# Kernel optimization log

Hardware: AMD Instinct MI355X
Metric: run time of the kernel (lower is better)

The kernel has to match this reference:

```python
import jax, jax.numpy as jnp
import numpy as np
from jax import lax

N, T, H, E = 50000, 200, 128, 1600000


def setup_inputs() -> dict:
    key = jax.random.key(0)
    ks = jax.random.split(key, 32)
    s = 0.05
    inp = {}
    inp["lightcurve"] = jax.random.normal(ks[0], (N, T), dtype=jnp.float32)
    inp["edge_index"] = jax.random.randint(ks[1], (2, E), 0, N, dtype=jnp.int32)
    # LSTM layer 0 (input_dim=1) and layer 1 (input H), PyTorch gate order i,f,g,o
    inp["W_ih0"] = jax.random.normal(ks[2], (4 * H, 1), jnp.float32) * s
    inp["W_hh0"] = jax.random.normal(ks[3], (4 * H, H), jnp.float32) * s
    inp["b_ih0"] = jnp.zeros((4 * H,), jnp.float32)
    inp["b_hh0"] = jnp.zeros((4 * H,), jnp.float32)
    inp["W_ih1"] = jax.random.normal(ks[4], (4 * H, H), jnp.float32) * s
    inp["W_hh1"] = jax.random.normal(ks[5], (4 * H, H), jnp.float32) * s
    inp["b_ih1"] = jnp.zeros((4 * H,), jnp.float32)
    inp["b_hh1"] = jnp.zeros((4 * H,), jnp.float32)
    # 3 GCN conv layers + LayerNorms
    for i in range(3):
        inp[f"Wg{i}"] = jax.random.normal(ks[6 + i], (H, H), jnp.float32) * s
        inp[f"bg{i}"] = jnp.zeros((H,), jnp.float32)
        inp[f"gamma{i}"] = jnp.ones((H,), jnp.float32)
        inp[f"beta{i}"] = jnp.zeros((H,), jnp.float32)
    inp["W_out"] = jax.random.normal(ks[10], (H, 1), jnp.float32) * s
    inp["b_out"] = jnp.zeros((1,), jnp.float32)
    return inp


def _lstm_encode(x, W_ih0, W_hh0, b_ih0, b_hh0, W_ih1, W_hh1, b_ih1, b_hh1):
    # x: [N, T, 1] -> final hidden of layer 2: [N, H]. Both layers fused in one scan.
    n = x.shape[0]
    h = W_hh0.shape[1]

    def cell(xt, hs, cs, Wih, Whh, bih, bhh):
        g = xt @ Wih.T + hs @ Whh.T + (bih + bhh)
        i, f, gg, o = jnp.split(g, 4, axis=-1)
        cs = jax.nn.sigmoid(f) * cs + jax.nn.sigmoid(i) * jnp.tanh(gg)
        hs = jax.nn.sigmoid(o) * jnp.tanh(cs)
        return hs, cs

    def step(carry, x_t):
        h1, c1, h2, c2 = carry
        h1, c1 = cell(x_t, h1, c1, W_ih0, W_hh0, b_ih0, b_hh0)
        h2, c2 = cell(h1, h2, c2, W_ih1, W_hh1, b_ih1, b_hh1)
        return (h1, c1, h2, c2), None

    z = jnp.zeros((n, h), x.dtype)
    (_, _, h2, _), _ = lax.scan(step, (z, z, z, z), jnp.swapaxes(x, 0, 1))
    return h2


def _forward(lightcurve, W_ih0, W_hh0, b_ih0, b_hh0, W_ih1, W_hh1, b_ih1, b_hh1,
             Wg0, bg0, gamma0, beta0, Wg1, bg1, gamma1, beta1, Wg2, bg2, gamma2, beta2,
             W_out, b_out, edge_index):
    n = lightcurve.shape[0]
    h = _lstm_encode(lightcurve[..., None], W_ih0, W_hh0, b_ih0, b_hh0,
                     W_ih1, W_hh1, b_ih1, b_hh1)
    # GCN normalization (PyG GCNConv defaults: add self-loops, symmetric norm)
    loops = jnp.arange(n, dtype=edge_index.dtype)
    row = jnp.concatenate([edge_index[0], loops])  # source
    col = jnp.concatenate([edge_index[1], loops])  # target
    deg = jax.ops.segment_sum(jnp.ones_like(col, dtype=h.dtype), col, num_segments=n)
    dinv = lax.rsqrt(jnp.maximum(deg, 1.0))
    enorm = dinv[row] * dinv[col]  # [E+N]
    for Wg, bg, gm, bt in ((Wg0, bg0, gamma0, beta0), (Wg1, bg1, gamma1, beta1), (Wg2, bg2, gamma2, beta2)):
        h_prev = h
        msg = (h @ Wg)[row] * enorm[:, None]            # gather + scale
        h = jax.ops.segment_sum(msg, col, num_segments=n) + bg  # scatter-add
        mu = h.mean(-1, keepdims=True)                  # LayerNorm
        var = jnp.mean((h - mu) ** 2, axis=-1, keepdims=True)
        h = (h - mu) * lax.rsqrt(var + 1e-5) * gm + bt
        h = jax.nn.relu(h)
        h = h + h_prev  # dropout is identity in eval mode
    pooled = h.mean(axis=0, keepdims=True)  # [1, H]
    return pooled @ W_out + b_out           # [1, 1]


def reference(lightcurve, edge_index, W_ih0, W_hh0, b_ih0, b_hh0,
              W_ih1, W_hh1, b_ih1, b_hh1,
              Wg0, bg0, gamma0, beta0, Wg1, bg1, gamma1, beta1,
              Wg2, bg2, gamma2, beta2, W_out, b_out):
    return _forward(lightcurve, W_ih0, W_hh0, b_ih0, b_hh0, W_ih1, W_hh1, b_ih1, b_hh1,
                    Wg0, bg0, gamma0, beta0, Wg1, bg1, gamma1, beta1,
                    Wg2, bg2, gamma2, beta2, W_out, b_out, edge_index)
```

## Files before the change

kernel.cpp:

```cpp
#include <hip/hip_runtime.h>

#define NN 50000
#define TT 200
#define HH 128
#define EE 1600000

typedef _Float16 f16x8 __attribute__((ext_vector_type(8)));
typedef _Float16 f16x4 __attribute__((ext_vector_type(4)));
typedef __fp16 fp16x2 __attribute__((ext_vector_type(2)));
typedef float f32x4 __attribute__((ext_vector_type(4)));

__device__ __forceinline__ float sigf(float x) {
    return __builtin_amdgcn_rcpf(1.f + __expf(-x));
}
__device__ __forceinline__ float tanhf_(float x) {
    return 1.f - 2.f * __builtin_amdgcn_rcpf(__expf(2.f * x) + 1.f);
}
__device__ __forceinline__ f32x4 sig4(f32x4 x) {
    f32x4 r; r[0] = sigf(x[0]); r[1] = sigf(x[1]); r[2] = sigf(x[2]); r[3] = sigf(x[3]); return r;
}
__device__ __forceinline__ f32x4 tanh4(f32x4 x) {
    f32x4 r; r[0] = tanhf_(x[0]); r[1] = tanhf_(x[1]); r[2] = tanhf_(x[2]); r[3] = tanhf_(x[3]); return r;
}
__device__ __forceinline__ f32x4 splat4(float s) { f32x4 r = {s, s, s, s}; return r; }
__device__ __forceinline__ f16x4 pack4(f32x4 v) {
    struct P { fp16x2 lo, hi; } p;
    p.lo = __builtin_amdgcn_cvt_pkrtz(v[0], v[1]);
    p.hi = __builtin_amdgcn_cvt_pkrtz(v[2], v[3]);
    return __builtin_bit_cast(f16x4, p);
}

__global__ void pack_w(const float* __restrict__ W, _Float16* __restrict__ out) {
    int tile = blockIdx.x;
    int jn = tile >> 2, kk = tile & 3;
    int L = threadIdx.x;
    int n = jn * 16 + (L & 15);
    int k0 = kk * 32 + (L >> 4) * 8;
    _Float16* dst = out + (size_t)tile * 512 + L * 8;
#pragma unroll
    for (int i = 0; i < 8; ++i) dst[i] = (_Float16)W[n * 128 + k0 + i];
}

__global__ void bias_prep(const float* __restrict__ bih0, const float* __restrict__ bhh0,
                          const float* __restrict__ bih1, const float* __restrict__ bhh1,
                          const float* __restrict__ wih0,
                          float* __restrict__ b0g, float* __restrict__ b1g, float* __restrict__ wxg) {
    int i = blockIdx.x * 256 + threadIdx.x;
    if (i < 512) {
        b0g[i] = bih0[i] + bhh0[i];
        b1g[i] = bih1[i] + bhh1[i];
        wxg[i] = wih0[i];
    }
}

__global__ void transpose_lc(const float* __restrict__ lc, float* __restrict__ xT) {
    __shared__ float tile[32][33];
    int tx = threadIdx.x, ty = threadIdx.y;
    int n0 = blockIdx.y * 32, t0 = blockIdx.x * 32;
#pragma unroll
    for (int i = 0; i < 32; i += 8) {
        int n = n0 + ty + i, t = t0 + tx;
        if (n < NN && t < TT) tile[ty + i][tx] = lc[(size_t)n * TT + t];
    }
    __syncthreads();
#pragma unroll
    for (int i = 0; i < 32; i += 8) {
        int t = t0 + ty + i, n = n0 + tx;
        if (n < NN && t < TT) xT[(size_t)t * NN + n] = tile[tx][ty + i];
    }
}


#define MFMA16(A, B, C) __builtin_amdgcn_mfma_f32_16x16x32_f16((A), (B), (C), 0, 0, 0)

#define MMCW(WB, HR, KK) {                                                      \
    const _Float16* wb_ = (WB) + (size_t)(KK) * 512 + lane * 8;                 \
    f16x8 wI_ = *reinterpret_cast<const f16x8*>(wb_ + (size_t)(0 * 8 + wj) * 2048); \
    f16x8 wF_ = *reinterpret_cast<const f16x8*>(wb_ + (size_t)(1 * 8 + wj) * 2048); \
    f16x8 wG_ = *reinterpret_cast<const f16x8*>(wb_ + (size_t)(2 * 8 + wj) * 2048); \
    f16x8 wO_ = *reinterpret_cast<const f16x8*>(wb_ + (size_t)(3 * 8 + wj) * 2048); \
    f16x8 h0_ = *reinterpret_cast<const f16x8*>(&(HR)[col][(KK) * 32 + quad * 8]);      \
    f16x8 h1_ = *reinterpret_cast<const f16x8*>(&(HR)[16 + col][(KK) * 32 + quad * 8]); \
    aI0 = MFMA16(wI_, h0_, aI0); aI1 = MFMA16(wI_, h1_, aI1);                   \
    aF0 = MFMA16(wF_, h0_, aF0); aF1 = MFMA16(wF_, h1_, aF1);                   \
    aG0 = MFMA16(wG_, h0_, aG0); aG1 = MFMA16(wG_, h1_, aG1);                   \
    aO0 = MFMA16(wO_, h0_, aO0); aO1 = MFMA16(wO_, h1_, aO1);                   \
}

#define EPIL0(NT, C, HV, AI, AF, AG, AO, XB) {                                  \
    f32x4 bI_ = *reinterpret_cast<const f32x4*>(&b0s[j0]);                      \
    f32x4 bF_ = *reinterpret_cast<const f32x4*>(&b0s[128 + j0]);                \
    f32x4 bG_ = *reinterpret_cast<const f32x4*>(&b0s[256 + j0]);                \
    f32x4 bO_ = *reinterpret_cast<const f32x4*>(&b0s[384 + j0]);                \
    f32x4 wIv_ = *reinterpret_cast<const f32x4*>(&wxs[j0]);                     \
    f32x4 wFv_ = *reinterpret_cast<const f32x4*>(&wxs[128 + j0]);               \
    f32x4 wGv_ = *reinterpret_cast<const f32x4*>(&wxs[256 + j0]);               \
    f32x4 wOv_ = *reinterpret_cast<const f32x4*>(&wxs[384 + j0]);               \
    f32x4 xv_ = splat4(xs[XB][(NT) * 16 + col]);                                \
    f32x4 gi_ = AI + bI_ + xv_ * wIv_;                                          \
    f32x4 gf_ = AF + bF_ + xv_ * wFv_;                                          \
    f32x4 gg_ = AG + bG_ + xv_ * wGv_;                                          \
    f32x4 go_ = AO + bO_ + xv_ * wOv_;                                          \
    C = sig4(gf_) * C + sig4(gi_) * tanh4(gg_);                                 \
    HV = sig4(go_) * tanh4(C);                                                  \
}

#define EPIL1(NT, C, HV, AI, AF, AG, AO) {                                      \
    f32x4 bI_ = *reinterpret_cast<const f32x4*>(&b1s[j0]);                      \
    f32x4 bF_ = *reinterpret_cast<const f32x4*>(&b1s[128 + j0]);                \
    f32x4 bG_ = *reinterpret_cast<const f32x4*>(&b1s[256 + j0]);                \
    f32x4 bO_ = *reinterpret_cast<const f32x4*>(&b1s[384 + j0]);                \
    f32x4 gi_ = AI + bI_;                                                       \
    f32x4 gf_ = AF + bF_;                                                       \
    f32x4 gg_ = AG + bG_;                                                       \
    f32x4 go_ = AO + bO_;                                                       \
    C = sig4(gf_) * C + sig4(gi_) * tanh4(gg_);                                 \
    HV = sig4(go_) * tanh4(C);                                                  \
}

#define WRHV(DST, NT, HV) \
    *reinterpret_cast<f16x4*>(&(DST)[(NT) * 16 + col][j0]) = pack4(HV);

__global__ __launch_bounds__(512, 2) void lstm_kernel(
    const float* __restrict__ xT,
    const _Float16* __restrict__ w0p,
    const _Float16* __restrict__ w1ip,
    const _Float16* __restrict__ w1hp,
    const float* __restrict__ b0g, const float* __restrict__ b1g,
    const float* __restrict__ wxg,
    float* __restrict__ h2out) {
    __shared__ _Float16 h1s[2][32][136];
    __shared__ _Float16 h2s[2][32][136];
    __shared__ __align__(16) float xs[2][32];
    __shared__ __align__(16) float b0s[512], b1s[512], wxs[512];

    const int tid = threadIdx.x;
    const int w = tid >> 6;
    const int wj = __builtin_amdgcn_readfirstlane(w);
    const int lane = tid & 63;
    const int col = lane & 15;
    const int quad = lane >> 4;
    const int n0 = blockIdx.x * 32;
    const int j0 = wj * 16 + quad * 4;

    for (int i = tid; i < 32 * 136; i += 512) (&h2s[1][0][0])[i] = (_Float16)0;
    if (tid < 512) { b0s[tid] = b0g[tid]; b1s[tid] = b1g[tid]; wxs[tid] = wxg[tid]; }
    if (tid < 32) {
        int n = n0 + tid;
        xs[0][tid] = (n < NN) ? xT[n] : 0.f;
        xs[1][tid] = (n < NN) ? xT[(size_t)NN + n] : 0.f;
    }

    f32x4 c1_0 = {}, c1_1 = {}, c2_0 = {}, c2_1 = {};

    __syncthreads();

    {
        f32x4 z = {};
        f32x4 h1v0, h1v1;
        EPIL0(0, c1_0, h1v0, z, z, z, z, 0)
        EPIL0(1, c1_1, h1v1, z, z, z, z, 0)
        WRHV(h1s[1], 0, h1v0)
        WRHV(h1s[1], 1, h1v1)
    }
    __syncthreads();

#pragma unroll 1
    for (int k = 0; k < TT - 1; ++k) {
        const int wp = k & 1;
        const int rp = wp ^ 1;
        _Float16 (*h1r)[136] = h1s[rp];
        _Float16 (*h2r)[136] = h2s[rp];
        _Float16 (*h1w)[136] = h1s[wp];
        _Float16 (*h2w)[136] = h2s[wp];
        {
            f32x4 aI0 = {}, aI1 = {}, aF0 = {}, aF1 = {};
            f32x4 aG0 = {}, aG1 = {}, aO0 = {}, aO1 = {};
            MMCW(w1ip, h1r, 0) MMCW(w1ip, h1r, 1) MMCW(w1ip, h1r, 2) MMCW(w1ip, h1r, 3)
            MMCW(w1hp, h2r, 0) MMCW(w1hp, h2r, 1) MMCW(w1hp, h2r, 2) MMCW(w1hp, h2r, 3)
            f32x4 h2v0, h2v1;
            EPIL1(0, c2_0, h2v0, aI0, aF0, aG0, aO0)
            EPIL1(1, c2_1, h2v1, aI1, aF1, aG1, aO1)
            WRHV(h2w, 0, h2v0)
            WRHV(h2w, 1, h2v1)
        }
        if (tid < 32) {
            int n_ = n0 + tid;
            float xv = 0.f;
            if (k + 2 < TT && n_ < NN) xv = xT[(size_t)(k + 2) * NN + n_];
            xs[wp][tid] = xv;
        }
        {
            f32x4 aI0 = {}, aI1 = {}, aF0 = {}, aF1 = {};
            f32x4 aG0 = {}, aG1 = {}, aO0 = {}, aO1 = {};
            MMCW(w0p, h1r, 0) MMCW(w0p, h1r, 1) MMCW(w0p, h1r, 2) MMCW(w0p, h1r, 3)
            f32x4 h1v0, h1v1;
            EPIL0(0, c1_0, h1v0, aI0, aF0, aG0, aO0, rp)
            EPIL0(1, c1_1, h1v1, aI1, aF1, aG1, aO1, rp)
            WRHV(h1w, 0, h1v0)
            WRHV(h1w, 1, h1v1)
        }
        __syncthreads();
    }

    {
        _Float16 (*h1r)[136] = h1s[0];
        _Float16 (*h2r)[136] = h2s[0];
        f32x4 aI0 = {}, aI1 = {}, aF0 = {}, aF1 = {};
        f32x4 aG0 = {}, aG1 = {}, aO0 = {}, aO1 = {};
        MMCW(w1ip, h1r, 0) MMCW(w1ip, h1r, 1) MMCW(w1ip, h1r, 2) MMCW(w1ip, h1r, 3)
        MMCW(w1hp, h2r, 0) MMCW(w1hp, h2r, 1) MMCW(w1hp, h2r, 2) MMCW(w1hp, h2r, 3)
        f32x4 h2v0, h2v1;
        EPIL1(0, c2_0, h2v0, aI0, aF0, aG0, aO0)
        EPIL1(1, c2_1, h2v1, aI1, aF1, aG1, aO1)
        int nA = n0 + col, nB = n0 + 16 + col;
        if (nA < NN) *reinterpret_cast<f32x4*>(&h2out[(size_t)nA * HH + j0]) = h2v0;
        if (nB < NN) *reinterpret_cast<f32x4*>(&h2out[(size_t)nB * HH + j0]) = h2v1;
    }
}

__global__ void deg_init(float* __restrict__ deg) {
    int i = blockIdx.x * 256 + threadIdx.x;
    if (i < NN) deg[i] = 1.f;
}
__global__ void deg_edges(const int* __restrict__ ei, float* __restrict__ deg) {
    int e = blockIdx.x * 256 + threadIdx.x;
    if (e < EE) unsafeAtomicAdd(&deg[ei[EE + e]], 1.f);
}
__global__ void dinv_k(const float* __restrict__ deg, float* __restrict__ dinv) {
    int i = blockIdx.x * 256 + threadIdx.x;
    if (i < NN) dinv[i] = rsqrtf(fmaxf(deg[i], 1.f));
}

__global__ void scan_off(const float* __restrict__ deg, int* __restrict__ off) {
    __shared__ int sp[256];
    const int tid = threadIdx.x;
    const int chunk = (NN + 255) / 256;
    const int i0 = tid * chunk;
    int s = 0;
    for (int i = 0; i < chunk; ++i) {
        int idx = i0 + i;
        if (idx < NN) s += (int)deg[idx] - 1;
    }
    sp[tid] = s;
    __syncthreads();
    for (int o = 1; o < 256; o <<= 1) {
        int v = (tid >= o) ? sp[tid - o] : 0;
        __syncthreads();
        sp[tid] += v;
        __syncthreads();
    }
    int run = sp[tid] - s;
    for (int i = 0; i < chunk; ++i) {
        int idx = i0 + i;
        if (idx < NN) { off[idx] = run; run += (int)deg[idx] - 1; }
    }
    if (tid == 255) off[NN] = sp[255];
}

__global__ void csr_fill(const int* __restrict__ ei, const float* __restrict__ dinv,
                         const int* __restrict__ off, int* __restrict__ cur,
                         int* __restrict__ crow, float* __restrict__ cw) {
    int e = blockIdx.x * 256 + threadIdx.x;
    if (e >= EE) return;
    int r = ei[e], c = ei[EE + e];
    int p = atomicAdd(&cur[c], 1);
    int idx = off[c] + p;
    crow[idx] = r;
    cw[idx] = dinv[r] * dinv[c];
}

__global__ void gcn_gemm(const float* __restrict__ h, const float* __restrict__ Wg,
                         float* __restrict__ hw) {
    __shared__ float hsT[128][36];
    int tid = threadIdx.x;
    int n0 = blockIdx.x * 32;
#pragma unroll
    for (int c = 0; c < 16; ++c) {
        int lin = c * 256 + tid;
        int m = lin >> 7, k = lin & 127;
        int n = n0 + m;
        hsT[k][m] = (n < NN) ? h[(size_t)n * HH + k] : 0.f;
    }
    __syncthreads();
    int j = tid & 127, p = tid >> 7;
    float acc[16];
#pragma unroll
    for (int m = 0; m < 16; ++m) acc[m] = 0.f;
    for (int k = 0; k < 128; ++k) {
        float wg = Wg[k * 128 + j];
        const float4* hp = reinterpret_cast<const float4*>(&hsT[k][p * 16]);
        float4 a = hp[0], b = hp[1], c = hp[2], d = hp[3];
        acc[0]  += a.x * wg; acc[1]  += a.y * wg; acc[2]  += a.z * wg; acc[3]  += a.w * wg;
        acc[4]  += b.x * wg; acc[5]  += b.y * wg; acc[6]  += b.z * wg; acc[7]  += b.w * wg;
        acc[8]  += c.x * wg; acc[9]  += c.y * wg; acc[10] += c.z * wg; acc[11] += c.w * wg;
        acc[12] += d.x * wg; acc[13] += d.y * wg; acc[14] += d.z * wg; acc[15] += d.w * wg;
    }
#pragma unroll
    for (int m = 0; m < 16; ++m) {
        int n = n0 + p * 16 + m;
        if (n < NN) hw[(size_t)n * HH + j] = acc[m];
    }
}

__global__ __launch_bounds__(256) void gcn_agg(
    const float* __restrict__ hw, const int* __restrict__ off,
    const int* __restrict__ crow, const float* __restrict__ cw,
    const float* __restrict__ dinv, const float* __restrict__ bg,
    const float* __restrict__ gamma, const float* __restrict__ beta,
    float* __restrict__ h) {
    __shared__ float xch[4][2];
    const int tid = threadIdx.x;
    const int half = tid >> 7;
    const int f = tid & 127;
    const int v = blockIdx.x * 2 + half;
    const float d = dinv[v];
    float acc = bg[f] + d * d * hw[v * HH + f];
    const int s1 = off[v + 1];
    for (int s = off[v]; s < s1; ++s) {
        int r = crow[s];
        float wv = cw[s];
        acc = fmaf(wv, hw[r * HH + f], acc);
    }
    float sum = acc, sq = acc * acc;
#pragma unroll
    for (int o = 32; o; o >>= 1) { sum += __shfl_xor(sum, o); sq += __shfl_xor(sq, o); }
    int wid = tid >> 6;
    if ((tid & 63) == 0) { xch[wid][0] = sum; xch[wid][1] = sq; }
    __syncthreads();
    sum += xch[wid ^ 1][0]; sq += xch[wid ^ 1][1];
    float mu = sum * (1.f / 128.f);
    float var = sq * (1.f / 128.f) - mu * mu;
    float rn = rsqrtf(var + 1e-5f);
    float o = (acc - mu) * rn * gamma[f] + beta[f];
    h[v * HH + f] = fmaxf(o, 0.f) + h[v * HH + f];
}

__global__ void pool_k(const float* __restrict__ h, float* __restrict__ pooled) {
    int j = threadIdx.x & 127, p = threadIdx.x >> 7;
    float s = 0.f;
    for (int n = blockIdx.x * 2 + p; n < NN; n += 512) s += h[(size_t)n * HH + j];
    unsafeAtomicAdd(&pooled[j], s);
}

__global__ void final_k(const float* __restrict__ pooled, const float* __restrict__ Wout,
                        const float* __restrict__ bout, float* __restrict__ out) {
    int lane = threadIdx.x;
    float s = pooled[lane] * Wout[lane] + pooled[lane + 64] * Wout[lane + 64];
#pragma unroll
    for (int o = 32; o; o >>= 1) s += __shfl_xor(s, o);
    if (lane == 0) out[0] = s * (1.f / (float)NN) + bout[0];
}

extern "C" void kernel_launch(void* const* d_in, const int* in_sizes, int n_in,
                              void* d_out, int out_size, void* d_ws, size_t ws_size,
                              hipStream_t stream) {
    const float* lc   = (const float*)d_in[0];
    const int*   ei   = (const int*)d_in[1];
    const float* Wih0 = (const float*)d_in[2];
    const float* Whh0 = (const float*)d_in[3];
    const float* bih0 = (const float*)d_in[4];
    const float* bhh0 = (const float*)d_in[5];
    const float* Wih1 = (const float*)d_in[6];
    const float* Whh1 = (const float*)d_in[7];
    const float* bih1 = (const float*)d_in[8];
    const float* bhh1 = (const float*)d_in[9];
    const float* Wout = (const float*)d_in[22];
    const float* bout = (const float*)d_in[23];
    float* out = (float*)d_out;

    float* ws   = (float*)d_ws;
    float* h    = ws;
    float* hw   = ws + 6400000;
    float* xT   = ws + 6400000;
    int*   off  = (int*)(ws + 12800000);
    int*   cur  = off + 50048;
    int*   crow = cur + 50048;
    float* cw   = (float*)(crow + EE);
    float* P      = ws + 16400064;
    float* deg    = P;
    float* dinv   = deg + 50000;
    float* b0g    = dinv + 50000;
    float* b1g    = b0g + 512;
    float* wxg    = b1g + 512;
    float* pooled = wxg + 512;
    _Float16* w0p  = (_Float16*)(pooled + 128);
    _Float16* w1ip = w0p + 65536;
    _Float16* w1hp = w1ip + 65536;

    pack_w<<<128, 64, 0, stream>>>(Whh0, w0p);
    pack_w<<<128, 64, 0, stream>>>(Wih1, w1ip);
    pack_w<<<128, 64, 0, stream>>>(Whh1, w1hp);
    bias_prep<<<2, 256, 0, stream>>>(bih0, bhh0, bih1, bhh1, Wih0, b0g, b1g, wxg);
    {
        dim3 g((TT + 31) / 32, (NN + 31) / 32), b(32, 8);
        transpose_lc<<<g, b, 0, stream>>>(lc, xT);
    }
    deg_init<<<(NN + 255) / 256, 256, 0, stream>>>(deg);
    deg_edges<<<(EE + 255) / 256, 256, 0, stream>>>(ei, deg);
    dinv_k<<<(NN + 255) / 256, 256, 0, stream>>>(deg, dinv);

    lstm_kernel<<<(NN + 31) / 32, 512, 0, stream>>>(xT, w0p, w1ip, w1hp, b0g, b1g, wxg, h);

    hipMemsetAsync(cur, 0, 50000 * sizeof(int), stream);
    scan_off<<<1, 256, 0, stream>>>(deg, off);
    csr_fill<<<(EE + 255) / 256, 256, 0, stream>>>(ei, dinv, off, cur, crow, cw);

    for (int l = 0; l < 3; ++l) {
        const float* Wg = (const float*)d_in[10 + 4 * l];
        const float* bg = (const float*)d_in[11 + 4 * l];
        const float* gm = (const float*)d_in[12 + 4 * l];
        const float* bt = (const float*)d_in[13 + 4 * l];
        gcn_gemm<<<(NN + 31) / 32, 256, 0, stream>>>(h, Wg, hw);
        gcn_agg<<<NN / 2, 256, 0, stream>>>(hw, off, crow, cw, dinv, bg, gm, bt, h);
    }

    hipMemsetAsync(pooled, 0, HH * sizeof(float), stream);
    pool_k<<<256, 256, 0, stream>>>(h, pooled);
    final_k<<<1, 64, 0, stream>>>(pooled, Wout, bout, out);
}
```

Measured before the change: 9.081 ms.

## Process 64 nodes per LSTM block to halve weight fetches per node

```diff
diff --git a/kernel.cpp b/kernel.cpp
--- a/kernel.cpp
+++ b/kernel.cpp
@@ -79,41 +79,35 @@
     f16x8 wF_ = *reinterpret_cast<const f16x8*>(wb_ + (size_t)(1 * 8 + wj) * 2048); \
     f16x8 wG_ = *reinterpret_cast<const f16x8*>(wb_ + (size_t)(2 * 8 + wj) * 2048); \
     f16x8 wO_ = *reinterpret_cast<const f16x8*>(wb_ + (size_t)(3 * 8 + wj) * 2048); \
-    f16x8 h0_ = *reinterpret_cast<const f16x8*>(&(HR)[col][(KK) * 32 + quad * 8]);      \
+    f16x8 h0_ = *reinterpret_cast<const f16x8*>(&(HR)[ 0 + col][(KK) * 32 + quad * 8]); \
     f16x8 h1_ = *reinterpret_cast<const f16x8*>(&(HR)[16 + col][(KK) * 32 + quad * 8]); \
+    f16x8 h2_ = *reinterpret_cast<const f16x8*>(&(HR)[32 + col][(KK) * 32 + quad * 8]); \
+    f16x8 h3_ = *reinterpret_cast<const f16x8*>(&(HR)[48 + col][(KK) * 32 + quad * 8]); \
     aI0 = MFMA16(wI_, h0_, aI0); aI1 = MFMA16(wI_, h1_, aI1);                   \
+    aI2 = MFMA16(wI_, h2_, aI2); aI3 = MFMA16(wI_, h3_, aI3);                   \
     aF0 = MFMA16(wF_, h0_, aF0); aF1 = MFMA16(wF_, h1_, aF1);                   \
+    aF2 = MFMA16(wF_, h2_, aF2); aF3 = MFMA16(wF_, h3_, aF3);                   \
     aG0 = MFMA16(wG_, h0_, aG0); aG1 = MFMA16(wG_, h1_, aG1);                   \
+    aG2 = MFMA16(wG_, h2_, aG2); aG3 = MFMA16(wG_, h3_, aG3);                   \
     aO0 = MFMA16(wO_, h0_, aO0); aO1 = MFMA16(wO_, h1_, aO1);                   \
+    aO2 = MFMA16(wO_, h2_, aO2); aO3 = MFMA16(wO_, h3_, aO3);                   \
 }
 
 #define EPIL0(NT, C, HV, AI, AF, AG, AO, XB) {                                  \
-    f32x4 bI_ = *reinterpret_cast<const f32x4*>(&b0s[j0]);                      \
-    f32x4 bF_ = *reinterpret_cast<const f32x4*>(&b0s[128 + j0]);                \
-    f32x4 bG_ = *reinterpret_cast<const f32x4*>(&b0s[256 + j0]);                \
-    f32x4 bO_ = *reinterpret_cast<const f32x4*>(&b0s[384 + j0]);                \
-    f32x4 wIv_ = *reinterpret_cast<const f32x4*>(&wxs[j0]);                     \
-    f32x4 wFv_ = *reinterpret_cast<const f32x4*>(&wxs[128 + j0]);               \
-    f32x4 wGv_ = *reinterpret_cast<const f32x4*>(&wxs[256 + j0]);               \
-    f32x4 wOv_ = *reinterpret_cast<const f32x4*>(&wxs[384 + j0]);               \
     f32x4 xv_ = splat4(xs[XB][(NT) * 16 + col]);                                \
-    f32x4 gi_ = AI + bI_ + xv_ * wIv_;                                          \
-    f32x4 gf_ = AF + bF_ + xv_ * wFv_;                                          \
-    f32x4 gg_ = AG + bG_ + xv_ * wGv_;                                          \
-    f32x4 go_ = AO + bO_ + xv_ * wOv_;                                          \
+    f32x4 gi_ = AI + bI0_ + xv_ * wIv_;                                         \
+    f32x4 gf_ = AF + bF0_ + xv_ * wFv_;                                         \
+    f32x4 gg_ = AG + bG0_ + xv_ * wGv_;                                         \
+    f32x4 go_ = AO + bO0_ + xv_ * wOv_;                                         \
     C = sig4(gf_) * C + sig4(gi_) * tanh4(gg_);                                 \
     HV = sig4(go_) * tanh4(C);                                                  \
 }
 
-#define EPIL1(NT, C, HV, AI, AF, AG, AO) {                                      \
-    f32x4 bI_ = *reinterpret_cast<const f32x4*>(&b1s[j0]);                      \
-    f32x4 bF_ = *reinterpret_cast<const f32x4*>(&b1s[128 + j0]);                \
-    f32x4 bG_ = *reinterpret_cast<const f32x4*>(&b1s[256 + j0]);                \
-    f32x4 bO_ = *reinterpret_cast<const f32x4*>(&b1s[384 + j0]);                \
-    f32x4 gi_ = AI + bI_;                                                       \
-    f32x4 gf_ = AF + bF_;                                                       \
-    f32x4 gg_ = AG + bG_;                                                       \
-    f32x4 go_ = AO + bO_;                                                       \
+#define EPIL1(C, HV, AI, AF, AG, AO) {                                          \
+    f32x4 gi_ = AI + bI1_;                                                      \
+    f32x4 gf_ = AF + bF1_;                                                      \
+    f32x4 gg_ = AG + bG1_;                                                      \
+    f32x4 go_ = AO + bO1_;                                                      \
     C = sig4(gf_) * C + sig4(gi_) * tanh4(gg_);                                 \
     HV = sig4(go_) * tanh4(C);                                                  \
 }
@@ -129,9 +123,9 @@
     const float* __restrict__ b0g, const float* __restrict__ b1g,
     const float* __restrict__ wxg,
     float* __restrict__ h2out) {
-    __shared__ _Float16 h1s[2][32][136];
-    __shared__ _Float16 h2s[2][32][136];
-    __shared__ __align__(16) float xs[2][32];
+    __shared__ _Float16 h1s[2][64][138];
+    __shared__ _Float16 h2s[2][64][138];
+    __shared__ __align__(16) float xs[2][64];
     __shared__ __align__(16) float b0s[512], b1s[512], wxs[512];
 
     const int tid = threadIdx.x;
@@ -140,28 +134,46 @@
     const int lane = tid & 63;
     const int col = lane & 15;
     const int quad = lane >> 4;
-    const int n0 = blockIdx.x * 32;
+    const int n0 = blockIdx.x * 64;
     const int j0 = wj * 16 + quad * 4;
 
-    for (int i = tid; i < 32 * 136; i += 512) (&h2s[1][0][0])[i] = (_Float16)0;
-    if (tid < 512) { b0s[tid] = b0g[tid]; b1s[tid] = b1g[tid]; wxs[tid] = wxg[tid]; }
-    if (tid < 32) {
+    for (int i = tid; i < 64 * 138; i += 512) (&h2s[1][0][0])[i] = (_Float16)0;
+    b0s[tid] = b0g[tid]; wxs[tid] = wxg[tid]; b1s[tid] = b1g[tid];
+    if (tid < 64) {
         int n = n0 + tid;
         xs[0][tid] = (n < NN) ? xT[n] : 0.f;
         xs[1][tid] = (n < NN) ? xT[(size_t)NN + n] : 0.f;
     }
 
-    f32x4 c1_0 = {}, c1_1 = {}, c2_0 = {}, c2_1 = {};
-
-    __syncthreads();
+    f32x4 c1_0 = {}, c1_1 = {}, c1_2 = {}, c1_3 = {};
+    f32x4 c2_0 = {}, c2_1 = {}, c2_2 = {}, c2_3 = {};
+
+    __syncthreads();
+
+    const f32x4 bI0_ = *reinterpret_cast<const f32x4*>(&b0s[j0]);
+    const f32x4 bF0_ = *reinterpret_cast<const f32x4*>(&b0s[128 + j0]);
+    const f32x4 bG0_ = *reinterpret_cast<const f32x4*>(&b0s[256 + j0]);
+    const f32x4 bO0_ = *reinterpret_cast<const f32x4*>(&b0s[384 + j0]);
+    const f32x4 wIv_ = *reinterpret_cast<const f32x4*>(&wxs[j0]);
+    const f32x4 wFv_ = *reinterpret_cast<const f32x4*>(&wxs[128 + j0]);
+    const f32x4 wGv_ = *reinterpret_cast<const f32x4*>(&wxs[256 + j0]);
+    const f32x4 wOv_ = *reinterpret_cast<const f32x4*>(&wxs[384 + j0]);
+    const f32x4 bI1_ = *reinterpret_cast<const f32x4*>(&b1s[j0]);
+    const f32x4 bF1_ = *reinterpret_cast<const f32x4*>(&b1s[128 + j0]);
+    const f32x4 bG1_ = *reinterpret_cast<const f32x4*>(&b1s[256 + j0]);
+    const f32x4 bO1_ = *reinterpret_cast<const f32x4*>(&b1s[384 + j0]);
 
     {
         f32x4 z = {};
-        f32x4 h1v0, h1v1;
+        f32x4 h1v0, h1v1, h1v2, h1v3;
         EPIL0(0, c1_0, h1v0, z, z, z, z, 0)
         EPIL0(1, c1_1, h1v1, z, z, z, z, 0)
+        EPIL0(2, c1_2, h1v2, z, z, z, z, 0)
+        EPIL0(3, c1_3, h1v3, z, z, z, z, 0)
         WRHV(h1s[1], 0, h1v0)
         WRHV(h1s[1], 1, h1v1)
+        WRHV(h1s[1], 2, h1v2)
+        WRHV(h1s[1], 3, h1v3)
     }
     __syncthreads();
 
@@ -169,53 +181,71 @@
     for (int k = 0; k < TT - 1; ++k) {
         const int wp = k & 1;
         const int rp = wp ^ 1;
-        _Float16 (*h1r)[136] = h1s[rp];
-        _Float16 (*h2r)[136] = h2s[rp];
-        _Float16 (*h1w)[136] = h1s[wp];
-        _Float16 (*h2w)[136] = h2s[wp];
+        _Float16 (*h1r)[138] = h1s[rp];
+        _Float16 (*h2r)[138] = h2s[rp];
+        _Float16 (*h1w)[138] = h1s[wp];
+        _Float16 (*h2w)[138] = h2s[wp];
         {
-            f32x4 aI0 = {}, aI1 = {}, aF0 = {}, aF1 = {};
-            f32x4 aG0 = {}, aG1 = {}, aO0 = {}, aO1 = {};
+            f32x4 aI0 = {}, aI1 = {}, aI2 = {}, aI3 = {};
+            f32x4 aF0 = {}, aF1 = {}, aF2 = {}, aF3 = {};
+            f32x4 aG0 = {}, aG1 = {}, aG2 = {}, aG3 = {};
+            f32x4 aO0 = {}, aO1 = {}, aO2 = {}, aO3 = {};
             MMCW(w1ip, h1r, 0) MMCW(w1ip, h1r, 1) MMCW(w1ip, h1r, 2) MMCW(w1ip, h1r, 3)
             MMCW(w1hp, h2r, 0) MMCW(w1hp, h2r, 1) MMCW(w1hp, h2r, 2) MMCW(w1hp, h2r, 3)
-            f32x4 h2v0, h2v1;
-            EPIL1(0, c2_0, h2v0, aI0, aF0, aG0, aO0)
-            EPIL1(1, c2_1, h2v1, aI1, aF1, aG1, aO1)
+            f32x4 h2v0, h2v1, h2v2, h2v3;
+            EPIL1(c2_0, h2v0, aI0, aF0, aG0, aO0)
+            EPIL1(c2_1, h2v1, aI1, aF1, aG1, aO1)
+            EPIL1(c2_2, h2v2, aI2, aF2, aG2, aO2)
+            EPIL1(c2_3, h2v3, aI3, aF3, aG3, aO3)
             WRHV(h2w, 0, h2v0)
             WRHV(h2w, 1, h2v1)
+            WRHV(h2w, 2, h2v2)
+            WRHV(h2w, 3, h2v3)
         }
-        if (tid < 32) {
+        if (tid < 64) {
             int n_ = n0 + tid;
             float xv = 0.f;
             if (k + 2 < TT && n_ < NN) xv = xT[(size_t)(k + 2) * NN + n_];
             xs[wp][tid] = xv;
         }
         {
-            f32x4 aI0 = {}, aI1 = {}, aF0 = {}, aF1 = {};
-            f32x4 aG0 = {}, aG1 = {}, aO0 = {}, aO1 = {};
+            f32x4 aI0 = {}, aI1 = {}, aI2 = {}, aI3 = {};
+            f32x4 aF0 = {}, aF1 = {}, aF2 = {}, aF3 = {};
+            f32x4 aG0 = {}, aG1 = {}, aG2 = {}, aG3 = {};
+            f32x4 aO0 = {}, aO1 = {}, aO2 = {}, aO3 = {};
             MMCW(w0p, h1r, 0) MMCW(w0p, h1r, 1) MMCW(w0p, h1r, 2) MMCW(w0p, h1r, 3)
-            f32x4 h1v0, h1v1;
+            f32x4 h1v0, h1v1, h1v2, h1v3;
             EPIL0(0, c1_0, h1v0, aI0, aF0, aG0, aO0, rp)
             EPIL0(1, c1_1, h1v1, aI1, aF1, aG1, aO1, rp)
+            EPIL0(2, c1_2, h1v2, aI2, aF2, aG2, aO2, rp)
+            EPIL0(3, c1_3, h1v3, aI3, aF3, aG3, aO3, rp)
             WRHV(h1w, 0, h1v0)
             WRHV(h1w, 1, h1v1)
+            WRHV(h1w, 2, h1v2)
+            WRHV(h1w, 3, h1v3)
         }
         __syncthreads();
     }
 
     {
-        _Float16 (*h1r)[136] = h1s[0];
-        _Float16 (*h2r)[136] = h2s[0];
-        f32x4 aI0 = {}, aI1 = {}, aF0 = {}, aF1 = {};
-        f32x4 aG0 = {}, aG1 = {}, aO0 = {}, aO1 = {};
+        _Float16 (*h1r)[138] = h1s[0];
+        _Float16 (*h2r)[138] = h2s[0];
+        f32x4 aI0 = {}, aI1 = {}, aI2 = {}, aI3 = {};
+        f32x4 aF0 = {}, aF1 = {}, aF2 = {}, aF3 = {};
+        f32x4 aG0 = {}, aG1 = {}, aG2 = {}, aG3 = {};
+        f32x4 aO0 = {}, aO1 = {}, aO2 = {}, aO3 = {};
         MMCW(w1ip, h1r, 0) MMCW(w1ip, h1r, 1) MMCW(w1ip, h1r, 2) MMCW(w1ip, h1r, 3)
         MMCW(w1hp, h2r, 0) MMCW(w1hp, h2r, 1) MMCW(w1hp, h2r, 2) MMCW(w1hp, h2r, 3)
-        f32x4 h2v0, h2v1;
-        EPIL1(0, c2_0, h2v0, aI0, aF0, aG0, aO0)
-        EPIL1(1, c2_1, h2v1, aI1, aF1, aG1, aO1)
-        int nA = n0 + col, nB = n0 + 16 + col;
+        f32x4 h2v0, h2v1, h2v2, h2v3;
+        EPIL1(c2_0, h2v0, aI0, aF0, aG0, aO0)
+        EPIL1(c2_1, h2v1, aI1, aF1, aG1, aO1)
+        EPIL1(c2_2, h2v2, aI2, aF2, aG2, aO2)
+        EPIL1(c2_3, h2v3, aI3, aF3, aG3, aO3)
+        int nA = n0 + col, nB = n0 + 16 + col, nC = n0 + 32 + col, nD = n0 + 48 + col;
         if (nA < NN) *reinterpret_cast<f32x4*>(&h2out[(size_t)nA * HH + j0]) = h2v0;
         if (nB < NN) *reinterpret_cast<f32x4*>(&h2out[(size_t)nB * HH + j0]) = h2v1;
+        if (nC < NN) *reinterpret_cast<f32x4*>(&h2out[(size_t)nC * HH + j0]) = h2v2;
+        if (nD < NN) *reinterpret_cast<f32x4*>(&h2out[(size_t)nD * HH + j0]) = h2v3;
     }
 }
 
@@ -400,7 +430,7 @@
     deg_edges<<<(EE + 255) / 256, 256, 0, stream>>>(ei, deg);
     dinv_k<<<(NN + 255) / 256, 256, 0, stream>>>(deg, dinv);
 
-    lstm_kernel<<<(NN + 31) / 32, 512, 0, stream>>>(xT, w0p, w1ip, w1hp, b0g, b1g, wxg, h);
+    lstm_kernel<<<(NN + 63) / 64, 512, 0, stream>>>(xT, w0p, w1ip, w1hp, b0g, b1g, wxg, h);
 
     hipMemsetAsync(cur, 0, 50000 * sizeof(int), stream);
     scan_off<<<1, 256, 0, stream>>>(deg, off);
```

New measurement: 16.53 ms. +82.0%, slower.
